# Kernel tuning notes

Hardware: AMD Instinct MI355X
Metric: run time of the kernel (lower is better)

Reference implementation:

```python
import jax, jax.numpy as jnp
import numpy as np

NUM_EXPERTS = 64
NUM_SELECTED = 2
HASH_BITS = 32


def setup_inputs() -> dict:
    key = jax.random.key(0)
    k1, k2 = jax.random.split(key)
    hidden_states = jax.random.normal(k1, (4, 4096, 2048), dtype=jnp.float32)
    # torch Linear weight [out_features, in_features], init normal(std=0.01), bias zeros
    hash_w = jax.random.normal(k2, (NUM_SELECTED * HASH_BITS, 2048), dtype=jnp.float32) * 0.01
    hash_b = jnp.zeros((NUM_SELECTED * HASH_BITS,), dtype=jnp.float32)
    return {"hidden_states": hidden_states, "hash_w": hash_w, "hash_b": hash_b}


def reference(hidden_states, hash_w, hash_b):
    B, S, H = hidden_states.shape
    T = B * S
    x = hidden_states.reshape(T, H)
    # hash projection: [T, k*32]
    h = x @ hash_w.T + hash_b
    bits = (h > 0).astype(jnp.int32).reshape(T, NUM_SELECTED, HASH_BITS)
    cand = bits.sum(axis=-1) % NUM_EXPERTS  # [T, k] candidate expert per slot

    # Sequential dedup (vectorized over tokens): for each slot i in order, if the
    # candidate collides with an already-chosen expert for that token, advance
    # (e+1) % E until a free expert is found (always exists since k <= E).
    used = jnp.zeros((T, NUM_EXPERTS), dtype=bool)
    offs = jnp.arange(NUM_EXPERTS)
    chosen = []
    for i in range(NUM_SELECTED):
        e = cand[:, i]  # [T]
        pos = (e[:, None] + offs[None, :]) % NUM_EXPERTS  # [T, E] probe sequence
        probed = jnp.take_along_axis(used, pos, axis=1)  # [T, E] used flags along probe
        off = jnp.argmax(~probed, axis=1)  # first free offset (0 if candidate free)
        ne = (e + off) % NUM_EXPERTS
        used = used | jax.nn.one_hot(ne, NUM_EXPERTS, dtype=bool)
        chosen.append(ne)
    expert_indices = jnp.stack(chosen, axis=1).astype(jnp.int32)  # [T, k]
    expert_weights = jnp.full((T, NUM_SELECTED), 1.0 / NUM_SELECTED, dtype=jnp.float32)
    router_logits = jnp.zeros((T, NUM_EXPERTS), dtype=jnp.float32)
    return expert_weights, expert_indices, router_logits
```

## Files before the change

### kernel.cpp

```cpp
#include <hip/hip_runtime.h>


constexpr int H_DIM  = 2048;
constexpr int NJ     = 64;
constexpr int TOK    = 16;
constexpr int KC     = 64;
constexpr int NCHUNK = H_DIM / KC;
constexpr int XF     = TOK * KC;
constexpr int WF     = NJ * KC;
constexpr int BUF    = XF + WF;
constexpr int XSLOTS = XF / 4;
constexpr int NTHR   = 256;
constexpr int SLOTS  = BUF / 4;

__device__ __forceinline__ int sw_of(int row) {
    return (3 * (row >> 3) + ((row >> 2) & 1)) & 7;
}

__device__ __forceinline__ void stage_chunk(const float* __restrict__ x,
                                            const float* __restrict__ w,
                                            float* smem, int fb,
                                            int tok0, int k0, int tid) {
#pragma unroll
    for (int it = 0; it < SLOTS / NTHR; ++it) {
        const int slot = it * NTHR + tid;
        const float* g;
        if (slot < XSLOTS) {
            const int row = slot >> 4, c4p = slot & 15;
            g = x + (size_t)(tok0 + row) * H_DIM + k0 + ((c4p ^ sw_of(row)) << 2);
        } else {
            const int s2 = slot - XSLOTS;
            const int row = s2 >> 4, c4p = s2 & 15;
            g = w + (size_t)row * H_DIM + k0 + ((c4p ^ sw_of(row)) << 2);
        }
        __builtin_amdgcn_global_load_lds(
            (const __attribute__((address_space(1))) void*)g,
            (__attribute__((address_space(3))) void*)(smem + fb + slot * 4),
            16, 0, 0);
    }
}

__global__ __launch_bounds__(NTHR, 2) void hash_router_kernel(
    const float* __restrict__ x,
    const float* __restrict__ w,
    const float* __restrict__ b,
    float* __restrict__ out,
    int T)
{
    __shared__ float smem[2 * BUF];
    unsigned int* bitw = (unsigned int*)(smem + 2048);

    const int tid = threadIdx.x;
    const int og  = tid & 7;
    const int tg  = (tid >> 3) & 1;
    const int kg  = tid >> 4;
    const int tok0 = blockIdx.x * TOK;

    float acc[8][8];
#pragma unroll
    for (int i = 0; i < 8; ++i)
#pragma unroll
        for (int j = 0; j < 8; ++j) acc[i][j] = 0.f;

    stage_chunk(x, w, smem, 0, tok0, 0, tid);

    for (int ch = 0; ch < NCHUNK; ++ch) {
        __builtin_amdgcn_s_waitcnt(0x0f70);
        __syncthreads();
        if (ch + 1 < NCHUNK)
            stage_chunk(x, w, smem, ((ch + 1) & 1) * BUF, tok0, (ch + 1) * KC, tid);

        const int fb = (ch & 1) * BUF;
        const int k4 = kg;
        float4 xv[8];
#pragma unroll
        for (int i = 0; i < 8; ++i) {
            const int row = tg * 8 + i;
            xv[i] = *(const float4*)(smem + fb + row * KC + ((k4 ^ sw_of(row)) << 2));
        }
#pragma unroll
        for (int j = 0; j < 8; ++j) {
            const int row = og * 8 + j;
            const float4 wv = *(const float4*)(smem + fb + XF + row * KC + ((k4 ^ sw_of(row)) << 2));
#pragma unroll
            for (int i = 0; i < 8; ++i) {
                acc[i][j] += xv[i].x * wv.x;
                acc[i][j] += xv[i].y * wv.y;
                acc[i][j] += xv[i].z * wv.z;
                acc[i][j] += xv[i].w * wv.w;
            }
        }
    }

    __syncthreads();
#pragma unroll
    for (int i = 0; i < 8; ++i)
#pragma unroll
        for (int j = 0; j < 8; ++j) {
            acc[i][j] += __shfl_xor(acc[i][j], 16, 64);
            acc[i][j] += __shfl_xor(acc[i][j], 32, 64);
        }

    const int v    = tid >> 6;
    const int lane = tid & 63;
    const bool red = lane < 16;
    const int s    = tid & 15;
    const int sw   = s & 7;
#define ACC_PACK(f4) make_float4(acc[(f4) >> 1][((f4) & 1) * 4],     \
                                 acc[(f4) >> 1][((f4) & 1) * 4 + 1], \
                                 acc[(f4) >> 1][((f4) & 1) * 4 + 2], \
                                 acc[(f4) >> 1][((f4) & 1) * 4 + 3])
#define ACC_ADD(f4, val) { acc[(f4) >> 1][((f4) & 1) * 4]     += (val).x; \
                           acc[(f4) >> 1][((f4) & 1) * 4 + 1] += (val).y; \
                           acc[(f4) >> 1][((f4) & 1) * 4 + 2] += (val).z; \
                           acc[(f4) >> 1][((f4) & 1) * 4 + 3] += (val).w; }
    if (v >= 2 && red) {
        float* base = smem + ((v - 2) * 16 + s) * 64;
#pragma unroll
        for (int f4 = 0; f4 < 16; ++f4) *(float4*)(base + ((f4 ^ sw) << 2)) = ACC_PACK(f4);
    }
    if (v == 0 && lane >= 16 && lane < 48) bitw[lane - 16] = 0u;
    __syncthreads();
    if (v < 2 && red) {
        const float* base = smem + (v * 16 + s) * 64;
#pragma unroll
        for (int f4 = 0; f4 < 16; ++f4) { float4 t = *(const float4*)(base + ((f4 ^ sw) << 2)); ACC_ADD(f4, t); }
    }
    __syncthreads();
    if (v == 1 && red) {
        float* base = smem + s * 64;
#pragma unroll
        for (int f4 = 0; f4 < 16; ++f4) *(float4*)(base + ((f4 ^ sw) << 2)) = ACC_PACK(f4);
    }
    __syncthreads();

    if (v == 0 && red) {
        const float* base = smem + s * 64;
#pragma unroll
        for (int f4 = 0; f4 < 16; ++f4) { float4 t = *(const float4*)(base + ((f4 ^ sw) << 2)); ACC_ADD(f4, t); }

        float bias[8];
#pragma unroll
        for (int j = 0; j < 8; ++j) bias[j] = b[og * 8 + j];

        const float TH = 5e-5f;
#pragma unroll
        for (int i = 0; i < 8; ++i) {
            unsigned int byte = 0u;
#pragma unroll
            for (int j = 0; j < 8; ++j) {
                const float hv = acc[i][j] + bias[j];
                bool pos;
                if (__builtin_expect(fabsf(hv) < TH, 0)) {
                    const float* xr = x + (size_t)(tok0 + tg * 8 + i) * H_DIM;
                    const float* wr = w + (size_t)(og * 8 + j) * H_DIM;
                    double sd = (double)bias[j];
                    for (int k = 0; k < H_DIM; ++k)
                        sd += (double)xr[k] * (double)wr[k];
                    pos = (sd > 0.0);
                } else {
                    pos = (hv > 0.0f);
                }
                byte |= (pos ? 1u : 0u) << j;
            }
            if (byte) atomicOr(&bitw[(tg * 8 + i) * 2 + (og >> 2)], byte << ((og & 3) * 8));
        }
    }
    __syncthreads();

    if (tid < TOK) {
        const int t  = tok0 + tid;
        const int c0 = __popc(bitw[tid * 2 + 0]);
        const int c1 = __popc(bitw[tid * 2 + 1]);
        const int i1 = c1 + ((c1 == c0) ? 1 : 0);
        float2 wq; wq.x = 0.5f; wq.y = 0.5f;
        *(float2*)(out + 2 * (size_t)t) = wq;
        float2 iq; iq.x = (float)c0; iq.y = (float)i1;
        *(float2*)(out + 2 * (size_t)T + 2 * (size_t)t) = iq;
    }

    float4 z; z.x = 0.f; z.y = 0.f; z.z = 0.f; z.w = 0.f;
    float* lbase = out + 4 * (size_t)T + (size_t)tok0 * NJ;
#pragma unroll
    for (int i = tid; i < TOK * NJ / 4; i += NTHR)
        *(float4*)(lbase + i * 4) = z;
}

extern "C" void kernel_launch(void* const* d_in, const int* in_sizes, int n_in,
                              void* d_out, int out_size, void* d_ws, size_t ws_size,
                              hipStream_t stream) {
    const float* x = (const float*)d_in[0];
    const float* w = (const float*)d_in[1];
    const float* b = (const float*)d_in[2];
    float* out = (float*)d_out;
    const int T = in_sizes[0] / H_DIM;
    const int grid = T / TOK;
    hash_router_kernel<<<dim3(grid), dim3(NTHR), 0, stream>>>(x, w, b, out, T);
}
```

Baseline: 320.4 us.

## Replace FP32 FMA GEMM with split-bf16 MFMA and direct global loads

Replaces the LDS-staged FP32 FMA projection with 16x16x32 bf16 MFMA instructions. Each fp32 operand is split into a hi and a lo bf16 pair, and three MFMAs per tile recover near-fp32 accuracy. Operands now load straight from global memory with no LDS staging, and K is split across the four waves with an LDS reduction at the end. Bit counting uses wave ballots instead of shared atomics. The kernel remains bound by streaming x from memory, and small accuracy differences are handled by the existing fp64 fallback for near-zero values.

```diff
diff --git a/kernel.cpp b/kernel.cpp
--- a/kernel.cpp
+++ b/kernel.cpp
@@ -3,187 +3,147 @@
 
 constexpr int H_DIM  = 2048;
 constexpr int NJ     = 64;
-constexpr int TOK    = 16;
-constexpr int KC     = 64;
-constexpr int NCHUNK = H_DIM / KC;
-constexpr int XF     = TOK * KC;
-constexpr int WF     = NJ * KC;
-constexpr int BUF    = XF + WF;
-constexpr int XSLOTS = XF / 4;
-constexpr int NTHR   = 256;
-constexpr int SLOTS  = BUF / 4;
+constexpr int TOKB   = 16;
+constexpr int KW     = 512;
+constexpr int KSTEPS = KW / 32;
 
-__device__ __forceinline__ int sw_of(int row) {
-    return (3 * (row >> 3) + ((row >> 2) & 1)) & 7;
+typedef __attribute__((ext_vector_type(8))) short  bf16x8;
+typedef __attribute__((ext_vector_type(4))) float  f32x4;
+
+__device__ __forceinline__ unsigned int bf16rne(float f) {
+    unsigned int u = __float_as_uint(f);
+    return (u + 0x7FFFu + ((u >> 16) & 1u)) >> 16;
 }
 
-__device__ __forceinline__ void stage_chunk(const float* __restrict__ x,
-                                            const float* __restrict__ w,
-                                            float* smem, int fb,
-                                            int tok0, int k0, int tid) {
-#pragma unroll
-    for (int it = 0; it < SLOTS / NTHR; ++it) {
-        const int slot = it * NTHR + tid;
-        const float* g;
-        if (slot < XSLOTS) {
-            const int row = slot >> 4, c4p = slot & 15;
-            g = x + (size_t)(tok0 + row) * H_DIM + k0 + ((c4p ^ sw_of(row)) << 2);
-        } else {
-            const int s2 = slot - XSLOTS;
-            const int row = s2 >> 4, c4p = s2 & 15;
-            g = w + (size_t)row * H_DIM + k0 + ((c4p ^ sw_of(row)) << 2);
-        }
-        __builtin_amdgcn_global_load_lds(
-            (const __attribute__((address_space(1))) void*)g,
-            (__attribute__((address_space(3))) void*)(smem + fb + slot * 4),
-            16, 0, 0);
-    }
+__device__ __forceinline__ void split8(const f32x4 a0, const f32x4 a1,
+                                       bf16x8& hi, bf16x8& lo) {
+    union { bf16x8 v; unsigned int u[4]; } H, L;
+    const unsigned int u0 = __float_as_uint(a0.x), u1 = __float_as_uint(a0.y);
+    const unsigned int u2 = __float_as_uint(a0.z), u3 = __float_as_uint(a0.w);
+    const unsigned int u4 = __float_as_uint(a1.x), u5 = __float_as_uint(a1.y);
+    const unsigned int u6 = __float_as_uint(a1.z), u7 = __float_as_uint(a1.w);
+    H.u[0] = (u0 >> 16) | (u1 & 0xFFFF0000u);
+    H.u[1] = (u2 >> 16) | (u3 & 0xFFFF0000u);
+    H.u[2] = (u4 >> 16) | (u5 & 0xFFFF0000u);
+    H.u[3] = (u6 >> 16) | (u7 & 0xFFFF0000u);
+    const float l0 = a0.x - __uint_as_float(u0 & 0xFFFF0000u);
+    const float l1 = a0.y - __uint_as_float(u1 & 0xFFFF0000u);
+    const float l2 = a0.z - __uint_as_float(u2 & 0xFFFF0000u);
+    const float l3 = a0.w - __uint_as_float(u3 & 0xFFFF0000u);
+    const float l4 = a1.x - __uint_as_float(u4 & 0xFFFF0000u);
+    const float l5 = a1.y - __uint_as_float(u5 & 0xFFFF0000u);
+    const float l6 = a1.z - __uint_as_float(u6 & 0xFFFF0000u);
+    const float l7 = a1.w - __uint_as_float(u7 & 0xFFFF0000u);
+    L.u[0] = bf16rne(l0) | (bf16rne(l1) << 16);
+    L.u[1] = bf16rne(l2) | (bf16rne(l3) << 16);
+    L.u[2] = bf16rne(l4) | (bf16rne(l5) << 16);
+    L.u[3] = bf16rne(l6) | (bf16rne(l7) << 16);
+    hi = H.v; lo = L.v;
 }
 
-__global__ __launch_bounds__(NTHR, 2) void hash_router_kernel(
+__global__ __launch_bounds__(256, 2) void hash_mfma_kernel(
     const float* __restrict__ x,
     const float* __restrict__ w,
     const float* __restrict__ b,
     float* __restrict__ out,
     int T)
 {
-    __shared__ float smem[2 * BUF];
-    unsigned int* bitw = (unsigned int*)(smem + 2048);
+    __shared__ float red[3 * 64 * 16];
 
-    const int tid = threadIdx.x;
-    const int og  = tid & 7;
-    const int tg  = (tid >> 3) & 1;
-    const int kg  = tid >> 4;
-    const int tok0 = blockIdx.x * TOK;
+    const int tid  = threadIdx.x;
+    const int wv   = tid >> 6;
+    const int lane = tid & 63;
+    const int row  = lane & 15;
+    const int kq   = lane >> 4;
+    const int tokB = blockIdx.x * TOKB;
 
-    float acc[8][8];
+    const float* xA = x + (size_t)(tokB + row) * H_DIM + wv * KW + kq * 8;
+    const float* wB = w + (size_t)row * H_DIM + wv * KW + kq * 8;
+
+    f32x4 acc[4];
 #pragma unroll
-    for (int i = 0; i < 8; ++i)
-#pragma unroll
-        for (int j = 0; j < 8; ++j) acc[i][j] = 0.f;
+    for (int jt = 0; jt < 4; ++jt) acc[jt] = (f32x4){0.f, 0.f, 0.f, 0.f};
 
-    stage_chunk(x, w, smem, 0, tok0, 0, tid);
-
-    for (int ch = 0; ch < NCHUNK; ++ch) {
-        __builtin_amdgcn_s_waitcnt(0x0f70);
-        __syncthreads();
-        if (ch + 1 < NCHUNK)
-            stage_chunk(x, w, smem, ((ch + 1) & 1) * BUF, tok0, (ch + 1) * KC, tid);
-
-        const int fb = (ch & 1) * BUF;
-        const int k4 = kg;
-        float4 xv[8];
-#pragma unroll
-        for (int i = 0; i < 8; ++i) {
-            const int row = tg * 8 + i;
-            xv[i] = *(const float4*)(smem + fb + row * KC + ((k4 ^ sw_of(row)) << 2));
+#pragma unroll 2
+    for (int ks = 0; ks < KSTEPS; ++ks) {
+        const int k0 = ks * 32;
+        bf16x8 AH, AL;
+        {
+            const f32x4 a0 = *(const f32x4*)(xA + k0);
+            const f32x4 a1 = *(const f32x4*)(xA + k0 + 4);
+            split8(a0, a1, AH, AL);
         }
 #pragma unroll
-        for (int j = 0; j < 8; ++j) {
-            const int row = og * 8 + j;
-            const float4 wv = *(const float4*)(smem + fb + XF + row * KC + ((k4 ^ sw_of(row)) << 2));
-#pragma unroll
-            for (int i = 0; i < 8; ++i) {
-                acc[i][j] += xv[i].x * wv.x;
-                acc[i][j] += xv[i].y * wv.y;
-                acc[i][j] += xv[i].z * wv.z;
-                acc[i][j] += xv[i].w * wv.w;
-            }
+        for (int jt = 0; jt < 4; ++jt) {
+            const float* wp = wB + (size_t)jt * 16 * H_DIM + k0;
+            const f32x4 b0 = *(const f32x4*)(wp);
+            const f32x4 b1 = *(const f32x4*)(wp + 4);
+            bf16x8 BH, BL;
+            split8(b0, b1, BH, BL);
+            acc[jt] = __builtin_amdgcn_mfma_f32_16x16x32_bf16(AL, BH, acc[jt], 0, 0, 0);
+            acc[jt] = __builtin_amdgcn_mfma_f32_16x16x32_bf16(AH, BL, acc[jt], 0, 0, 0);
+            acc[jt] = __builtin_amdgcn_mfma_f32_16x16x32_bf16(AH, BH, acc[jt], 0, 0, 0);
         }
     }
 
-    __syncthreads();
+    if (wv) {
+        float* rp = red + ((wv - 1) * 64 + lane) * 16;
 #pragma unroll
-    for (int i = 0; i < 8; ++i)
-#pragma unroll
-        for (int j = 0; j < 8; ++j) {
-            acc[i][j] += __shfl_xor(acc[i][j], 16, 64);
-            acc[i][j] += __shfl_xor(acc[i][j], 32, 64);
-        }
-
-    const int v    = tid >> 6;
-    const int lane = tid & 63;
-    const bool red = lane < 16;
-    const int s    = tid & 15;
-    const int sw   = s & 7;
-#define ACC_PACK(f4) make_float4(acc[(f4) >> 1][((f4) & 1) * 4],     \
-                                 acc[(f4) >> 1][((f4) & 1) * 4 + 1], \
-                                 acc[(f4) >> 1][((f4) & 1) * 4 + 2], \
-                                 acc[(f4) >> 1][((f4) & 1) * 4 + 3])
-#define ACC_ADD(f4, val) { acc[(f4) >> 1][((f4) & 1) * 4]     += (val).x; \
-                           acc[(f4) >> 1][((f4) & 1) * 4 + 1] += (val).y; \
-                           acc[(f4) >> 1][((f4) & 1) * 4 + 2] += (val).z; \
-                           acc[(f4) >> 1][((f4) & 1) * 4 + 3] += (val).w; }
-    if (v >= 2 && red) {
-        float* base = smem + ((v - 2) * 16 + s) * 64;
-#pragma unroll
-        for (int f4 = 0; f4 < 16; ++f4) *(float4*)(base + ((f4 ^ sw) << 2)) = ACC_PACK(f4);
-    }
-    if (v == 0 && lane >= 16 && lane < 48) bitw[lane - 16] = 0u;
-    __syncthreads();
-    if (v < 2 && red) {
-        const float* base = smem + (v * 16 + s) * 64;
-#pragma unroll
-        for (int f4 = 0; f4 < 16; ++f4) { float4 t = *(const float4*)(base + ((f4 ^ sw) << 2)); ACC_ADD(f4, t); }
-    }
-    __syncthreads();
-    if (v == 1 && red) {
-        float* base = smem + s * 64;
-#pragma unroll
-        for (int f4 = 0; f4 < 16; ++f4) *(float4*)(base + ((f4 ^ sw) << 2)) = ACC_PACK(f4);
+        for (int jt = 0; jt < 4; ++jt) *(f32x4*)(rp + jt * 4) = acc[jt];
     }
     __syncthreads();
 
-    if (v == 0 && red) {
-        const float* base = smem + s * 64;
+    if (wv == 0) {
 #pragma unroll
-        for (int f4 = 0; f4 < 16; ++f4) { float4 t = *(const float4*)(base + ((f4 ^ sw) << 2)); ACC_ADD(f4, t); }
+        for (int w2 = 0; w2 < 3; ++w2)
+#pragma unroll
+            for (int jt = 0; jt < 4; ++jt) {
+                const f32x4 t = *(const f32x4*)(red + (w2 * 64 + lane) * 16 + jt * 4);
+                acc[jt].x += t.x; acc[jt].y += t.y; acc[jt].z += t.z; acc[jt].w += t.w;
+            }
 
-        float bias[8];
+        float bias[4];
 #pragma unroll
-        for (int j = 0; j < 8; ++j) bias[j] = b[og * 8 + j];
+        for (int jt = 0; jt < 4; ++jt) bias[jt] = b[jt * 16 + row];
 
         const float TH = 5e-5f;
+        int c0 = 0, c1 = 0;
+        const int myg = (lane >> 2) & 3;
+        const int myr = lane & 3;
 #pragma unroll
-        for (int i = 0; i < 8; ++i) {
-            unsigned int byte = 0u;
+        for (int jt = 0; jt < 4; ++jt)
 #pragma unroll
-            for (int j = 0; j < 8; ++j) {
-                const float hv = acc[i][j] + bias[j];
+            for (int r = 0; r < 4; ++r) {
+                const float h = acc[jt][r] + bias[jt];
                 bool pos;
-                if (__builtin_expect(fabsf(hv) < TH, 0)) {
-                    const float* xr = x + (size_t)(tok0 + tg * 8 + i) * H_DIM;
-                    const float* wr = w + (size_t)(og * 8 + j) * H_DIM;
-                    double sd = (double)bias[j];
+                if (__builtin_expect(fabsf(h) < TH, 0)) {
+                    const float* xr = x + (size_t)(tokB + (lane >> 4) * 4 + r) * H_DIM;
+                    const float* wr = w + (size_t)(jt * 16 + row) * H_DIM;
+                    double sd = (double)bias[jt];
                     for (int k = 0; k < H_DIM; ++k)
                         sd += (double)xr[k] * (double)wr[k];
                     pos = (sd > 0.0);
                 } else {
-                    pos = (hv > 0.0f);
+                    pos = (h > 0.0f);
                 }
-                byte |= (pos ? 1u : 0u) << j;
+                const unsigned long long bal = __ballot(pos);
+                const int add = ((myr == r) ? 1 : 0) *
+                    __popc((unsigned int)((bal >> (myg * 16)) & 0xFFFFu));
+                if (jt < 2) c0 += add; else c1 += add;
             }
-            if (byte) atomicOr(&bitw[(tg * 8 + i) * 2 + (og >> 2)], byte << ((og & 3) * 8));
+
+        if (lane < TOKB) {
+            const int t  = tokB + lane;
+            const int i1 = c1 + ((c1 == c0) ? 1 : 0);
+            float2 wq; wq.x = 0.5f; wq.y = 0.5f;
+            *(float2*)(out + 2 * (size_t)t) = wq;
+            float2 iq; iq.x = (float)c0; iq.y = (float)i1;
+            *(float2*)(out + 2 * (size_t)T + 2 * (size_t)t) = iq;
         }
     }
-    __syncthreads();
 
-    if (tid < TOK) {
-        const int t  = tok0 + tid;
-        const int c0 = __popc(bitw[tid * 2 + 0]);
-        const int c1 = __popc(bitw[tid * 2 + 1]);
-        const int i1 = c1 + ((c1 == c0) ? 1 : 0);
-        float2 wq; wq.x = 0.5f; wq.y = 0.5f;
-        *(float2*)(out + 2 * (size_t)t) = wq;
-        float2 iq; iq.x = (float)c0; iq.y = (float)i1;
-        *(float2*)(out + 2 * (size_t)T + 2 * (size_t)t) = iq;
-    }
-
-    float4 z; z.x = 0.f; z.y = 0.f; z.z = 0.f; z.w = 0.f;
-    float* lbase = out + 4 * (size_t)T + (size_t)tok0 * NJ;
-#pragma unroll
-    for (int i = tid; i < TOK * NJ / 4; i += NTHR)
-        *(float4*)(lbase + i * 4) = z;
+    f32x4 z = (f32x4){0.f, 0.f, 0.f, 0.f};
+    *(f32x4*)(out + 4 * (size_t)T + (size_t)tokB * NJ + (size_t)tid * 4) = z;
 }
 
 extern "C" void kernel_launch(void* const* d_in, const int* in_sizes, int n_in,
@@ -194,6 +154,5 @@
     const float* b = (const float*)d_in[2];
     float* out = (float*)d_out;
     const int T = in_sizes[0] / H_DIM;
-    const int grid = T / TOK;
-    hash_router_kernel<<<dim3(grid), dim3(NTHR), 0, stream>>>(x, w, b, out, T);
+    hash_mfma_kernel<<<dim3(T / TOKB), dim3(256), 0, stream>>>(x, w, b, out, T);
 }
```

Measured after the change: 313.4 us. -2.2%, faster.
